# Kernel tuning notes

Hardware: AMD Instinct MI355X
Metric: run time of the kernel (lower is better)

## Reference

```python
import jax, jax.numpy as jnp
import numpy as np

VOCAB = 32000
HID = 1024


def setup_inputs() -> dict:
    key = jax.random.key(0)
    ks = jax.random.split(key, 6)
    B, S = 32, 1024
    x = jax.random.randint(ks[0], (B, S), 0, VOCAB, dtype=jnp.int64) if jax.config.jax_enable_x64 else jax.random.randint(ks[0], (B, S), 0, VOCAB, dtype=jnp.int32)
    scale = 1.0 / np.sqrt(HID)
    embed = jax.random.normal(ks[1], (VOCAB, HID), dtype=jnp.float32) * scale
    embed = embed.at[0].set(0.0)  # padding_idx=0
    Wc = jax.random.normal(ks[2], (HID, HID), dtype=jnp.float32) * scale
    bc = jnp.zeros((HID,), dtype=jnp.float32)
    Wgx = jax.random.normal(ks[3], (HID, 3 * HID), dtype=jnp.float32) * scale
    # gate bias init: reset=2.0, persistence=2.0, accumulation=0.0
    bgx = jnp.concatenate([
        jnp.full((HID,), 2.0, dtype=jnp.float32),
        jnp.full((HID,), 2.0, dtype=jnp.float32),
        jnp.zeros((HID,), dtype=jnp.float32),
    ])
    Wgh = jax.random.normal(ks[4], (HID, 3 * HID), dtype=jnp.float32) * scale
    return {"x": x, "embed": embed, "Wc": Wc, "bc": bc, "Wgx": Wgx, "bgx": bgx, "Wgh": Wgh}


def reference(x, embed, Wc, bc, Wgx, bgx, Wgh):
    # x: (B,S) int token ids
    B, S = x.shape
    H = HID
    e = embed[x]  # (B,S,H)  dropout is identity in eval mode
    gate_x = jnp.einsum('bsh,hg->bsg', e, Wgx) + bgx       # (B,S,3H)
    cand = jnp.tanh(jnp.einsum('bsh,hk->bsk', e, Wc) + bc)  # (B,S,H)

    def step(h, inputs):
        gx_t, v_t = inputs  # (B,3H), (B,H)
        gates = jax.nn.sigmoid(gx_t + h @ Wgh)  # (B,3H)
        rho = gates[:, :H]
        pi = gates[:, H:2 * H]
        alpha = gates[:, 2 * H:]
        h_new = rho * (pi * h + alpha * v_t)
        return h_new, None

    h0 = jnp.zeros((B, H), dtype=e.dtype)
    h_final, _ = jax.lax.scan(step, h0, (jnp.swapaxes(gate_x, 0, 1), jnp.swapaxes(cand, 0, 1)))
    return h_final  # (B,H)
```

## Files before the change

kernel.cpp:

```cpp
#include <hip/hip_runtime.h>
#include <cstdint>
#include <cstddef>

#define HID   1024
#define BATCH 32
#define SEQ   1024
#define NROWS 32768
#define G3    3072
#define NWG   128
#define NFLAGS ((SEQ + 1) * NWG)
#define HSLOT 32768

typedef __attribute__((ext_vector_type(8))) short bf16x8_t;
typedef __attribute__((ext_vector_type(4))) float f32x4_t;

__device__ __forceinline__ unsigned short f2bf(float f) {
  unsigned u = __float_as_uint(f);
  u += 0x7FFFu + ((u >> 16) & 1u);
  return (unsigned short)(u >> 16);
}
__device__ __forceinline__ float bf2f(unsigned short s) {
  return __uint_as_float(((unsigned)s) << 16);
}

__device__ __forceinline__ void store_short_wt(unsigned short* p, unsigned short v) {
  asm volatile("global_store_short %0, %1, off sc0 sc1"
               :: "v"(p), "v"((unsigned)v) : "memory");
}

__global__ __launch_bounds__(256) void transpose_cast(const float* __restrict__ in,
                                                      unsigned short* __restrict__ out,
                                                      int N) {
  __shared__ float tile[32][33];
  int k0 = blockIdx.x * 32, n0 = blockIdx.y * 32;
  int tx = threadIdx.x, ty = threadIdx.y;
#pragma unroll
  for (int i = 0; i < 4; ++i)
    tile[ty + 8 * i][tx] = in[(size_t)(k0 + ty + 8 * i) * N + n0 + tx];
  __syncthreads();
#pragma unroll
  for (int i = 0; i < 4; ++i)
    out[(size_t)(n0 + ty + 8 * i) * HID + k0 + tx] = f2bf(tile[tx][ty + 8 * i]);
}

__global__ __launch_bounds__(256) void gather_cast(const int* __restrict__ x,
                                                   const float* __restrict__ embed,
                                                   unsigned short* __restrict__ e) {
  int r = blockIdx.x;
  int t = threadIdx.x;
  int tok = x[r];
  const float4* src = (const float4*)(embed + (size_t)tok * HID);
  float4 v = src[t];
  ushort4 o;
  o.x = f2bf(v.x); o.y = f2bf(v.y); o.z = f2bf(v.z); o.w = f2bf(v.w);
  ((ushort4*)(e + (size_t)r * HID))[t] = o;
}

__global__ __launch_bounds__(256) void gemm_fused(const unsigned short* __restrict__ A,
                                                  const unsigned short* __restrict__ B,
                                                  const float* __restrict__ bgx,
                                                  const float* __restrict__ bc,
                                                  unsigned short* __restrict__ gx,
                                                  unsigned short* __restrict__ cand) {
  __shared__ unsigned short As[128 * 32];
  __shared__ unsigned short Bs[128 * 32];
  const int bm = blockIdx.x * 128, bn = blockIdx.y * 128;
  const int t = threadIdx.x;
  const int wave = t >> 6, lane = t & 63;
  const int q = lane >> 4, nidx = lane & 15;
  const int wm = (wave & 1) * 64, wn = (wave >> 1) * 64;
  const int sr = t >> 2;
  const int kofs = (t & 3) * 8;

  f32x4_t acc[4][4];
#pragma unroll
  for (int i = 0; i < 4; ++i)
#pragma unroll
    for (int j = 0; j < 4; ++j) acc[i][j] = (f32x4_t){0.f, 0.f, 0.f, 0.f};

#pragma unroll 1
  for (int kt = 0; kt < HID; kt += 32) {
    __syncthreads();
#pragma unroll
    for (int c = 0; c < 2; ++c) {
      int row = c * 64 + sr;
      *(uint4*)(&As[row * 32 + kofs]) = *(const uint4*)(&A[(size_t)(bm + row) * HID + kt + kofs]);
      *(uint4*)(&Bs[row * 32 + kofs]) = *(const uint4*)(&B[(size_t)(bn + row) * HID + kt + kofs]);
    }
    __syncthreads();
    bf16x8_t af[4], bfr[4];
#pragma unroll
    for (int i = 0; i < 4; ++i)
      af[i] = *(const bf16x8_t*)(&As[(wm + i * 16 + nidx) * 32 + q * 8]);
#pragma unroll
    for (int j = 0; j < 4; ++j)
      bfr[j] = *(const bf16x8_t*)(&Bs[(wn + j * 16 + nidx) * 32 + q * 8]);
#pragma unroll
    for (int i = 0; i < 4; ++i)
#pragma unroll
      for (int j = 0; j < 4; ++j)
        acc[i][j] = __builtin_amdgcn_mfma_f32_16x16x32_bf16(af[i], bfr[j], acc[i][j], 0, 0, 0);
  }

#pragma unroll
  for (int i = 0; i < 4; ++i) {
#pragma unroll
    for (int j = 0; j < 4; ++j) {
#pragma unroll
      for (int reg = 0; reg < 4; ++reg) {
        int m = bm + wm + i * 16 + q * 4 + reg;
        int n = bn + wn + j * 16 + nidx;
        float v = acc[i][j][reg];
        if (n < G3) {
          gx[(size_t)m * G3 + n] = f2bf(v + bgx[n]);
        } else {
          int nc = n - G3;
          cand[(size_t)m * HID + nc] = f2bf(tanhf(v + bc[nc]));
        }
      }
    }
  }
}

__global__ __launch_bounds__(256) void init_state(unsigned int* __restrict__ flags,
                                                  unsigned short* __restrict__ ring) {
  int t = blockIdx.x * 256 + threadIdx.x;
  if (t < NFLAGS) flags[t] = (t < NWG) ? 1u : 0u;
  if (t < HSLOT) ring[t] = 0;
}

__global__ __launch_bounds__(128) void recurrence(const unsigned short* __restrict__ gx,
                                                  const unsigned short* __restrict__ cand,
                                                  const unsigned short* __restrict__ WghT,
                                                  unsigned short* __restrict__ ring,
                                                  unsigned int* __restrict__ flags,
                                                  float* __restrict__ out) {
  const int g = blockIdx.x;
  const int tid = threadIdx.x;
  const int w = tid >> 6;
  const int lane = tid & 63;
  const int q = lane >> 4, n = lane & 15;

  __shared__ __align__(16) unsigned short Bs[32 * 1024];

  for (int it = tid; it < 4096; it += 128) {
    int row = it >> 7, c16 = it & 127;
    int tile = row >> 4, rr = row & 15;
    uint4 val = {0u, 0u, 0u, 0u};
    if (tile == 0) {
      int gr = (rr < 8) ? (8 * g + rr) : (1024 + 8 * g + (rr - 8));
      val = ((const uint4*)(WghT + (size_t)gr * HID))[c16];
    } else if (rr < 8) {
      int gr = 2048 + 8 * g + rr;
      val = ((const uint4*)(WghT + (size_t)gr * HID))[c16];
    }
    *(uint4*)((char*)Bs + (size_t)(row * 128 + (c16 ^ (row & 7))) * 16) = val;
  }
  __syncthreads();

  __builtin_amdgcn_fence(__ATOMIC_ACQUIRE, "agent");

  float h_own[4] = {0.f, 0.f, 0.f, 0.f};
  const int c_rp = (n < 8) ? (8 * g + n) : (1024 + 8 * g + (n - 8));
  const int c_al = 2048 + 8 * g + (n & 7);
  const int c_h  = 8 * g + (n & 7);

  const char* b0p = (const char*)Bs + (size_t)n * 2048;
  const char* b1p = b0p + 16 * 2048;

#pragma unroll 1
  for (int t = 0; t < SEQ; ++t) {
    const unsigned short* hc = ring + ((size_t)t << 15);
    unsigned short* hn = ring + ((size_t)(t + 1) << 15);

    float g0v[4], g1v[4], vv[4];
#pragma unroll
    for (int r = 0; r < 4; ++r) {
      size_t rb = ((size_t)(w * 16 + q * 4 + r) * SEQ + t);
      g0v[r] = bf2f(gx[rb * G3 + c_rp]);
      g1v[r] = bf2f(gx[rb * G3 + c_al]);
      vv[r]  = bf2f(cand[rb * HID + c_h]);
    }

    const unsigned int* frow = flags + (size_t)t * NWG;
    while (__hip_atomic_load(&frow[tid], __ATOMIC_RELAXED, __HIP_MEMORY_SCOPE_AGENT) == 0u) {}
    __syncthreads();
    asm volatile("" ::: "memory");

    f32x4_t acc0 = (f32x4_t){0.f, 0.f, 0.f, 0.f};
    f32x4_t acc1 = (f32x4_t){0.f, 0.f, 0.f, 0.f};
    const unsigned short* ha = hc + (size_t)(w * 16 + n) * HID + q * 8;
#pragma unroll 8
    for (int kt = 0; kt < 32; ++kt) {
      bf16x8_t a = *(const bf16x8_t*)(ha + kt * 32);
      int sw = ((kt * 4 + q) ^ (n & 7)) * 16;
      bf16x8_t b0 = *(const bf16x8_t*)(b0p + sw);
      bf16x8_t b1 = *(const bf16x8_t*)(b1p + sw);
      acc0 = __builtin_amdgcn_mfma_f32_16x16x32_bf16(a, b0, acc0, 0, 0, 0);
      acc1 = __builtin_amdgcn_mfma_f32_16x16x32_bf16(a, b1, acc1, 0, 0, 0);
    }

#pragma unroll
    for (int r = 0; r < 4; ++r) {
      float s0 = 1.f / (1.f + __expf(-(acc0[r] + g0v[r])));
      float al = 1.f / (1.f + __expf(-(acc1[r] + g1v[r])));
      float piv = __shfl(s0, q * 16 + 8 + (n & 7), 64);
      if (n < 8) {
        h_own[r] = s0 * (piv * h_own[r] + al * vv[r]);
        store_short_wt(&hn[(size_t)(w * 16 + q * 4 + r) * HID + c_h], f2bf(h_own[r]));
      }
    }

    asm volatile("s_waitcnt vmcnt(0)" ::: "memory");
    __syncthreads();
    if (tid == 0)
      __hip_atomic_store(&flags[(size_t)(t + 1) * NWG + g], 1u,
                         __ATOMIC_RELAXED, __HIP_MEMORY_SCOPE_AGENT);
  }

#pragma unroll
  for (int r = 0; r < 4; ++r)
    if (n < 8)
      out[(size_t)(w * 16 + q * 4 + r) * HID + c_h] = h_own[r];
}

extern "C" void kernel_launch(void* const* d_in, const int* in_sizes, int n_in,
                              void* d_out, int out_size, void* d_ws, size_t ws_size,
                              hipStream_t stream) {
  const int*   x     = (const int*)d_in[0];
  const float* embed = (const float*)d_in[1];
  const float* Wc    = (const float*)d_in[2];
  const float* bc    = (const float*)d_in[3];
  const float* Wgx   = (const float*)d_in[4];
  const float* bgx   = (const float*)d_in[5];
  const float* Wgh   = (const float*)d_in[6];
  float* out = (float*)d_out;

  char* base = (char*)d_ws;
  unsigned short* e    = (unsigned short*)(base);
  unsigned short* Bp   = (unsigned short*)(base + 67108864);
  unsigned short* WghT = (unsigned short*)(base + 75497472);
  unsigned short* gxb  = (unsigned short*)(base + 81788928);
  unsigned short* cnd  = (unsigned short*)(base + 283115520);
  unsigned short* ring  = (unsigned short*)(base);
  unsigned int*   flags = (unsigned int*)(base + 350224384);

  transpose_cast<<<dim3(32, 96), dim3(32, 8), 0, stream>>>(Wgx, Bp, G3);
  transpose_cast<<<dim3(32, 32), dim3(32, 8), 0, stream>>>(Wc, Bp + (size_t)G3 * HID, HID);
  transpose_cast<<<dim3(32, 96), dim3(32, 8), 0, stream>>>(Wgh, WghT, G3);

  gather_cast<<<dim3(NROWS), dim3(256), 0, stream>>>(x, embed, e);

  gemm_fused<<<dim3(256, 32), dim3(256), 0, stream>>>(e, Bp, bgx, bc, gxb, cnd);

  init_state<<<dim3(513), dim3(256), 0, stream>>>(flags, ring);

  void* args[] = {(void*)&gxb, (void*)&cnd, (void*)&WghT, (void*)&ring,
                  (void*)&flags, (void*)&out};
  hipLaunchCooperativeKernel((const void*)recurrence, dim3(NWG), dim3(128), args, 0, stream);
}
```

Measured before the change: 6.307 ms.

## Halve recurrence workgroups, per-wave flags, and repack gate inputs per workgroup per step

The recurrence now uses 64 workgroups that each own 16 hidden columns. Reset and persistence weights stay in LDS, while the alpha weights are streamed from global memory for a third MFMA. Synchronisation moves from a per-workgroup flag with barriers to per-wave flags, so each lane polls one producer wave and the __syncthreads calls are gone. The GEMM epilogue writes gate and candidate values in a [t][wg] blocked layout, so each step's inputs are read contiguously. The trade-off is fewer workgroups, each doing more MFMA work per step, plus repeated global reads of the alpha weights.

```diff
diff --git a/kernel.cpp b/kernel.cpp
--- a/kernel.cpp
+++ b/kernel.cpp
@@ -7,9 +7,9 @@
 #define SEQ   1024
 #define NROWS 32768
 #define G3    3072
-#define NWG   128
-#define NFLAGS ((SEQ + 1) * NWG)
-#define HSLOT 32768
+#define NWG   64
+#define FLSTR 1025
+#define NFLAGS (128 * FLSTR)
 
 typedef __attribute__((ext_vector_type(8))) short bf16x8_t;
 typedef __attribute__((ext_vector_type(4))) float f32x4_t;
@@ -60,8 +60,8 @@
                                                   const unsigned short* __restrict__ B,
                                                   const float* __restrict__ bgx,
                                                   const float* __restrict__ bc,
-                                                  unsigned short* __restrict__ gx,
-                                                  unsigned short* __restrict__ cand) {
+                                                  unsigned short* __restrict__ gxp,
+                                                  unsigned short* __restrict__ cndp) {
   __shared__ unsigned short As[128 * 32];
   __shared__ unsigned short Bs[128 * 32];
   const int bm = blockIdx.x * 128, bn = blockIdx.y * 128;
@@ -110,12 +110,14 @@
       for (int reg = 0; reg < 4; ++reg) {
         int m = bm + wm + i * 16 + q * 4 + reg;
         int n = bn + wn + j * 16 + nidx;
+        int b = m >> 10, tt = m & 1023;
         float v = acc[i][j][reg];
         if (n < G3) {
-          gx[(size_t)m * G3 + n] = f2bf(v + bgx[n]);
+          int gate = n >> 10, colw = n & 1023, g2 = colw >> 4, c = colw & 15;
+          gxp[((size_t)tt * NWG + g2) * 1536 + gate * 512 + b * 16 + c] = f2bf(v + bgx[n]);
         } else {
-          int nc = n - G3;
-          cand[(size_t)m * HID + nc] = f2bf(tanhf(v + bc[nc]));
+          int cw = n - G3, g2 = cw >> 4, c = cw & 15;
+          cndp[((size_t)tt * NWG + g2) * 512 + b * 16 + c] = f2bf(tanhf(v + bc[cw]));
         }
       }
     }
@@ -125,12 +127,15 @@
 __global__ __launch_bounds__(256) void init_state(unsigned int* __restrict__ flags,
                                                   unsigned short* __restrict__ ring) {
   int t = blockIdx.x * 256 + threadIdx.x;
-  if (t < NFLAGS) flags[t] = (t < NWG) ? 1u : 0u;
-  if (t < HSLOT) ring[t] = 0;
-}
-
-__global__ __launch_bounds__(128) void recurrence(const unsigned short* __restrict__ gx,
-                                                  const unsigned short* __restrict__ cand,
+  if (t < NFLAGS) {
+    int rem = t - (t / FLSTR) * FLSTR;
+    flags[t] = (rem == 0) ? 1u : 0u;
+  }
+  if (t < BATCH * HID) ring[t] = 0;
+}
+
+__global__ __launch_bounds__(128) void recurrence(const unsigned short* __restrict__ gxp,
+                                                  const unsigned short* __restrict__ cndp,
                                                   const unsigned short* __restrict__ WghT,
                                                   unsigned short* __restrict__ ring,
                                                   unsigned int* __restrict__ flags,
@@ -145,15 +150,8 @@
 
   for (int it = tid; it < 4096; it += 128) {
     int row = it >> 7, c16 = it & 127;
-    int tile = row >> 4, rr = row & 15;
-    uint4 val = {0u, 0u, 0u, 0u};
-    if (tile == 0) {
-      int gr = (rr < 8) ? (8 * g + rr) : (1024 + 8 * g + (rr - 8));
-      val = ((const uint4*)(WghT + (size_t)gr * HID))[c16];
-    } else if (rr < 8) {
-      int gr = 2048 + 8 * g + rr;
-      val = ((const uint4*)(WghT + (size_t)gr * HID))[c16];
-    }
+    int gr = (row < 16) ? (16 * g + row) : (1024 + 16 * g + (row - 16));
+    uint4 val = ((const uint4*)(WghT + (size_t)gr * HID))[c16];
     *(uint4*)((char*)Bs + (size_t)(row * 128 + (c16 ^ (row & 7))) * 16) = val;
   }
   __syncthreads();
@@ -161,34 +159,35 @@
   __builtin_amdgcn_fence(__ATOMIC_ACQUIRE, "agent");
 
   float h_own[4] = {0.f, 0.f, 0.f, 0.f};
-  const int c_rp = (n < 8) ? (8 * g + n) : (1024 + 8 * g + (n - 8));
-  const int c_al = 2048 + 8 * g + (n & 7);
-  const int c_h  = 8 * g + (n & 7);
-
   const char* b0p = (const char*)Bs + (size_t)n * 2048;
   const char* b1p = b0p + 16 * 2048;
+  const unsigned short* alphaW = WghT + (size_t)(2048 + 16 * g + n) * HID + q * 8;
+  const unsigned int* fpoll = flags + (size_t)(lane * 2 + w) * FLSTR;
+  const int c_h = 16 * g + n;
 
 #pragma unroll 1
   for (int t = 0; t < SEQ; ++t) {
     const unsigned short* hc = ring + ((size_t)t << 15);
     unsigned short* hn = ring + ((size_t)(t + 1) << 15);
 
-    float g0v[4], g1v[4], vv[4];
+    const unsigned short* gblk = gxp + ((size_t)t * NWG + g) * 1536;
+    const unsigned short* cblk = cndp + ((size_t)t * NWG + g) * 512;
+    float g0v[4], g1v[4], g2v[4], vv[4];
 #pragma unroll
     for (int r = 0; r < 4; ++r) {
-      size_t rb = ((size_t)(w * 16 + q * 4 + r) * SEQ + t);
-      g0v[r] = bf2f(gx[rb * G3 + c_rp]);
-      g1v[r] = bf2f(gx[rb * G3 + c_al]);
-      vv[r]  = bf2f(cand[rb * HID + c_h]);
-    }
-
-    const unsigned int* frow = flags + (size_t)t * NWG;
-    while (__hip_atomic_load(&frow[tid], __ATOMIC_RELAXED, __HIP_MEMORY_SCOPE_AGENT) == 0u) {}
-    __syncthreads();
+      int b = w * 16 + q * 4 + r;
+      g0v[r] = bf2f(gblk[b * 16 + n]);
+      g1v[r] = bf2f(gblk[512 + b * 16 + n]);
+      g2v[r] = bf2f(gblk[1024 + b * 16 + n]);
+      vv[r]  = bf2f(cblk[b * 16 + n]);
+    }
+
+    while (__hip_atomic_load(&fpoll[t], __ATOMIC_RELAXED, __HIP_MEMORY_SCOPE_AGENT) == 0u) {}
     asm volatile("" ::: "memory");
 
     f32x4_t acc0 = (f32x4_t){0.f, 0.f, 0.f, 0.f};
     f32x4_t acc1 = (f32x4_t){0.f, 0.f, 0.f, 0.f};
+    f32x4_t acc2 = (f32x4_t){0.f, 0.f, 0.f, 0.f};
     const unsigned short* ha = hc + (size_t)(w * 16 + n) * HID + q * 8;
 #pragma unroll 8
     for (int kt = 0; kt < 32; ++kt) {
@@ -196,32 +195,30 @@
       int sw = ((kt * 4 + q) ^ (n & 7)) * 16;
       bf16x8_t b0 = *(const bf16x8_t*)(b0p + sw);
       bf16x8_t b1 = *(const bf16x8_t*)(b1p + sw);
+      bf16x8_t b2 = *(const bf16x8_t*)(alphaW + kt * 32);
       acc0 = __builtin_amdgcn_mfma_f32_16x16x32_bf16(a, b0, acc0, 0, 0, 0);
       acc1 = __builtin_amdgcn_mfma_f32_16x16x32_bf16(a, b1, acc1, 0, 0, 0);
+      acc2 = __builtin_amdgcn_mfma_f32_16x16x32_bf16(a, b2, acc2, 0, 0, 0);
     }
 
 #pragma unroll
     for (int r = 0; r < 4; ++r) {
-      float s0 = 1.f / (1.f + __expf(-(acc0[r] + g0v[r])));
-      float al = 1.f / (1.f + __expf(-(acc1[r] + g1v[r])));
-      float piv = __shfl(s0, q * 16 + 8 + (n & 7), 64);
-      if (n < 8) {
-        h_own[r] = s0 * (piv * h_own[r] + al * vv[r]);
-        store_short_wt(&hn[(size_t)(w * 16 + q * 4 + r) * HID + c_h], f2bf(h_own[r]));
-      }
+      float rho = 1.f / (1.f + __expf(-(acc0[r] + g0v[r])));
+      float pi  = 1.f / (1.f + __expf(-(acc1[r] + g1v[r])));
+      float al  = 1.f / (1.f + __expf(-(acc2[r] + g2v[r])));
+      h_own[r] = rho * (pi * h_own[r] + al * vv[r]);
+      store_short_wt(&hn[(size_t)(w * 16 + q * 4 + r) * HID + c_h], f2bf(h_own[r]));
     }
 
     asm volatile("s_waitcnt vmcnt(0)" ::: "memory");
-    __syncthreads();
-    if (tid == 0)
-      __hip_atomic_store(&flags[(size_t)(t + 1) * NWG + g], 1u,
+    if (lane == 0)
+      __hip_atomic_store(&flags[(size_t)(g * 2 + w) * FLSTR + t + 1], 1u,
                          __ATOMIC_RELAXED, __HIP_MEMORY_SCOPE_AGENT);
   }
 
 #pragma unroll
   for (int r = 0; r < 4; ++r)
-    if (n < 8)
-      out[(size_t)(w * 16 + q * 4 + r) * HID + c_h] = h_own[r];
+    out[(size_t)(w * 16 + q * 4 + r) * HID + c_h] = h_own[r];
 }
 
 extern "C" void kernel_launch(void* const* d_in, const int* in_sizes, int n_in,
@@ -240,10 +237,10 @@
   unsigned short* e    = (unsigned short*)(base);
   unsigned short* Bp   = (unsigned short*)(base + 67108864);
   unsigned short* WghT = (unsigned short*)(base + 75497472);
-  unsigned short* gxb  = (unsigned short*)(base + 81788928);
-  unsigned short* cnd  = (unsigned short*)(base + 283115520);
+  unsigned short* gxp  = (unsigned short*)(base + 81788928);
+  unsigned short* cndp = (unsigned short*)(base + 283115520);
   unsigned short* ring  = (unsigned short*)(base);
-  unsigned int*   flags = (unsigned int*)(base + 350224384);
+  unsigned int*   flags = (unsigned int*)(base + 70000000);
 
   transpose_cast<<<dim3(32, 96), dim3(32, 8), 0, stream>>>(Wgx, Bp, G3);
   transpose_cast<<<dim3(32, 32), dim3(32, 8), 0, stream>>>(Wc, Bp + (size_t)G3 * HID, HID);
@@ -251,11 +248,11 @@
 
   gather_cast<<<dim3(NROWS), dim3(256), 0, stream>>>(x, embed, e);
 
-  gemm_fused<<<dim3(256, 32), dim3(256), 0, stream>>>(e, Bp, bgx, bc, gxb, cnd);
+  gemm_fused<<<dim3(256, 32), dim3(256), 0, stream>>>(e, Bp, bgx, bc, gxp, cndp);
 
   init_state<<<dim3(513), dim3(256), 0, stream>>>(flags, ring);
 
-  void* args[] = {(void*)&gxb, (void*)&cnd, (void*)&WghT, (void*)&ring,
+  void* args[] = {(void*)&gxp, (void*)&cndp, (void*)&WghT, (void*)&ring,
                   (void*)&flags, (void*)&out};
   hipLaunchCooperativeKernel((const void*)recurrence, dim3(NWG), dim3(128), args, 0, stream);
 }
```

After: 10.12 ms. 60.4% more time.
